# Kernel optimization log

Hardware: AMD Instinct MI355X
Metric: run time of the kernel (lower is better)

The kernel has to match this reference:

```python
import jax, jax.numpy as jnp
import numpy as np

D_ATTN = 2048
D_STATE = 64
SHIFT_FRAC = 0.5
LN_EPS = 1e-5


def setup_inputs() -> dict:
    key = jax.random.key(0)
    ks = jax.random.split(key, 8)
    B, T = 8, 2048
    s_attn = 1.0 / np.sqrt(D_ATTN)
    s_state = 1.0 / np.sqrt(D_STATE)
    x = jax.random.normal(ks[0], (B, T, D_ATTN), jnp.float32)
    W_key = jax.random.normal(ks[1], (D_STATE, D_ATTN), jnp.float32) * s_attn
    W_value = jax.random.normal(ks[2], (D_STATE, D_ATTN), jnp.float32) * s_attn
    W_output = jax.random.normal(ks[3], (D_ATTN, D_STATE), jnp.float32) * s_state
    W_shift = jax.random.normal(ks[4], (D_ATTN, D_ATTN), jnp.float32) * s_attn
    gate = jnp.ones((D_ATTN,), jnp.float32)
    # negative decay log so w = exp(time_decay) in (e^-1, 1): stable over T=2048 steps
    time_decay = -jax.random.uniform(ks[5], (D_STATE,), jnp.float32, 0.05, 1.0)
    time_first = jax.random.normal(ks[6], (D_STATE,), jnp.float32) * 0.1
    ln_gamma = jnp.ones((D_ATTN,), jnp.float32)
    ln_beta = jnp.zeros((D_ATTN,), jnp.float32)
    return dict(x=x, W_key=W_key, W_value=W_value, W_output=W_output,
                W_shift=W_shift, gate=gate, time_decay=time_decay,
                time_first=time_first, ln_gamma=ln_gamma, ln_beta=ln_beta)


def reference(x, W_key, W_value, W_output, W_shift, gate, time_decay,
              time_first, ln_gamma, ln_beta):
    B, T, D = x.shape
    # token shift: cat([x[:, s:], x[:, :-s]], dim=1) == roll(x, -s, axis=1)
    shift_len = max(1, int(T * SHIFT_FRAC))
    x_cat = jnp.roll(x, -shift_len, axis=1)
    g = jax.nn.sigmoid(gate)
    x_shift = jnp.einsum('btd,ed->bte', x_cat, W_shift) * g + x * (1.0 - g)
    # LayerNorm over last dim
    mu = jnp.mean(x_shift, axis=-1, keepdims=True)
    var = jnp.var(x_shift, axis=-1, keepdims=True)
    x_norm = (x_shift - mu) * jax.lax.rsqrt(var + LN_EPS) * ln_gamma + ln_beta
    k = jnp.einsum('btd,sd->bts', x_norm, W_key)    # (B,T,Ds)
    v = jnp.einsum('btd,sd->bts', x_norm, W_value)  # (B,T,Ds)
    w = jnp.exp(time_decay)                          # (Ds,)
    u = jnp.exp(time_first)                          # (Ds,)
    wkv = jnp.exp(-u * jax.nn.sigmoid(k)) * v        # (B,T,Ds)
    # linear recurrence: state_t = w * state_{t-1} + wkv_t
    def step(state, wkv_t):
        state = state * w + wkv_t
        return state, state
    init = jnp.zeros((B, k.shape[-1]), x.dtype)
    last_state, states = jax.lax.scan(step, init, jnp.swapaxes(wkv, 0, 1))
    states = jnp.swapaxes(states, 0, 1)              # (B,T,Ds)
    # per-step output projection == single batched GEMM over stacked states
    output = jnp.einsum('bts,ds->btd', states, W_output)  # (B,T,D)
    # dropout in eval mode is identity; last_state is detached in original
    return output, jax.lax.stop_gradient(last_state)
```

## Files before the change

kernel.cpp:

```cpp
#include <hip/hip_runtime.h>
#include <stdint.h>

constexpr int kD  = 2048;
constexpr int kDS = 64;
constexpr int kNT = 2048;
constexpr int kM  = 8 * kNT;
constexpr int kOutElems = kM * kD;

typedef __attribute__((ext_vector_type(8))) short short8;
typedef __attribute__((ext_vector_type(8))) unsigned short bfu8;
typedef __attribute__((ext_vector_type(4))) unsigned short bfu4;
typedef __attribute__((ext_vector_type(4))) float f32x4;

__device__ __forceinline__ unsigned short f2bf(float f) {
  unsigned int u = __float_as_uint(f);
  return (unsigned short)((u + 0x7FFFu + ((u >> 16) & 1u)) >> 16);
}
__device__ __forceinline__ float bf2f(unsigned short b) {
  return __uint_as_float(((unsigned int)b) << 16);
}

__device__ __forceinline__ void gload16(const void* g, void* l) {
  __builtin_amdgcn_global_load_lds((__attribute__((address_space(1))) void*)g,
                                   (__attribute__((address_space(3))) void*)l,
                                   16, 0, 0);
}

__global__ void k_cvt(const float* __restrict__ src, unsigned short* __restrict__ dst, int n8) {
  int i8 = blockIdx.x * 256 + threadIdx.x;
  if (i8 >= n8) return;
  const f32x4* s = (const f32x4*)(src + (size_t)i8 * 8);
  f32x4 v0 = s[0], v1 = s[1];
  bfu8 o;
  o[0] = f2bf(v0[0]); o[1] = f2bf(v0[1]); o[2] = f2bf(v0[2]); o[3] = f2bf(v0[3]);
  o[4] = f2bf(v1[0]); o[5] = f2bf(v1[1]); o[6] = f2bf(v1[2]); o[7] = f2bf(v1[3]);
  *(bfu8*)(dst + (size_t)i8 * 8) = o;
}

__global__ void k_cvt_kv(const float* __restrict__ wk, const float* __restrict__ wv,
                         unsigned short* __restrict__ dst) {
  int i8 = blockIdx.x * 256 + threadIdx.x;
  int r = i8 >> 8;
  int dcol = (i8 & 255) << 3;
  int s = r >> 1;
  const float* src = (r & 1) ? wv : wk;
  const f32x4* p = (const f32x4*)(src + (size_t)s * kD + dcol);
  f32x4 v0 = p[0], v1 = p[1];
  bfu8 o;
  o[0] = f2bf(v0[0]); o[1] = f2bf(v0[1]); o[2] = f2bf(v0[2]); o[3] = f2bf(v0[3]);
  o[4] = f2bf(v1[0]); o[5] = f2bf(v1[1]); o[6] = f2bf(v1[2]); o[7] = f2bf(v1[3]);
  *(bfu8*)(dst + (size_t)i8 * 8) = o;
}

#define MM(x,y,z) __builtin_amdgcn_mfma_f32_16x16x32_bf16(x,y,z,0,0,0)
#define BAR __builtin_amdgcn_s_barrier()
#define WAITV_(N) asm volatile("s_waitcnt vmcnt(" #N ")" ::: "memory")
#define WAITV(N) WAITV_(N)
#define WAITL asm volatile("s_waitcnt lgkmcnt(0)")
#define NOWV (void)0

#define STAGEA_TO(BUF,H,Q,KT) gload16(aS + (size_t)(((H)*64+(Q)*128)*2048) + (KT), \
                                      smem + (BUF)*32768 + ((H)*64+(Q)*128)*64 + ldsAst)
#define STAGEB_TO(BUF,H,Q,KT) gload16(bS + (size_t)(((H)*32+(Q)*128)*2048) + (KT), \
                                      smem + (BUF)*32768 + 16384 + (H)*2048 + (Q)*8192 + ldsBst)

#define RDA(CUR,H,MF,KS) (*(const short8*)(smem + (CUR)*32768 + ardb + (H)*4096 + (MF)*1024 + colrd##KS))
#define RDB(CUR,H,NF,KS) (*(const short8*)(smem + (CUR)*32768 + 16384 + brdb + (H)*2048 + (NF)*1024 + colrd##KS))

#define RD_A(CUR,H) \
  a[0][0]=RDA(CUR,H,0,0); a[0][1]=RDA(CUR,H,0,1); \
  a[1][0]=RDA(CUR,H,1,0); a[1][1]=RDA(CUR,H,1,1); \
  a[2][0]=RDA(CUR,H,2,0); a[2][1]=RDA(CUR,H,2,1); \
  a[3][0]=RDA(CUR,H,3,0); a[3][1]=RDA(CUR,H,3,1)
#define RD_B(CUR,H,BV) \
  BV[0][0]=RDB(CUR,H,0,0); BV[0][1]=RDB(CUR,H,0,1); \
  BV[1][0]=RDB(CUR,H,1,0); BV[1][1]=RDB(CUR,H,1,1)

#define MF16(MH, B, NB) \
  __builtin_amdgcn_s_setprio(1); \
  acc[(MH)*4+0][(NB)+0] = MM(a[0][0], B[0][0], acc[(MH)*4+0][(NB)+0]); \
  acc[(MH)*4+0][(NB)+1] = MM(a[0][0], B[1][0], acc[(MH)*4+0][(NB)+1]); \
  acc[(MH)*4+1][(NB)+0] = MM(a[1][0], B[0][0], acc[(MH)*4+1][(NB)+0]); \
  acc[(MH)*4+1][(NB)+1] = MM(a[1][0], B[1][0], acc[(MH)*4+1][(NB)+1]); \
  acc[(MH)*4+2][(NB)+0] = MM(a[2][0], B[0][0], acc[(MH)*4+2][(NB)+0]); \
  acc[(MH)*4+2][(NB)+1] = MM(a[2][0], B[1][0], acc[(MH)*4+2][(NB)+1]); \
  acc[(MH)*4+3][(NB)+0] = MM(a[3][0], B[0][0], acc[(MH)*4+3][(NB)+0]); \
  acc[(MH)*4+3][(NB)+1] = MM(a[3][0], B[1][0], acc[(MH)*4+3][(NB)+1]); \
  acc[(MH)*4+0][(NB)+0] = MM(a[0][1], B[0][1], acc[(MH)*4+0][(NB)+0]); \
  acc[(MH)*4+0][(NB)+1] = MM(a[0][1], B[1][1], acc[(MH)*4+0][(NB)+1]); \
  acc[(MH)*4+1][(NB)+0] = MM(a[1][1], B[0][1], acc[(MH)*4+1][(NB)+0]); \
  acc[(MH)*4+1][(NB)+1] = MM(a[1][1], B[1][1], acc[(MH)*4+1][(NB)+1]); \
  acc[(MH)*4+2][(NB)+0] = MM(a[2][1], B[0][1], acc[(MH)*4+2][(NB)+0]); \
  acc[(MH)*4+2][(NB)+1] = MM(a[2][1], B[1][1], acc[(MH)*4+2][(NB)+1]); \
  acc[(MH)*4+3][(NB)+0] = MM(a[3][1], B[0][1], acc[(MH)*4+3][(NB)+0]); \
  acc[(MH)*4+3][(NB)+1] = MM(a[3][1], B[1][1], acc[(MH)*4+3][(NB)+1]); \
  __builtin_amdgcn_s_setprio(0)

#define PH0(CUR, S, KA1, WV) \
  BAR; WAITL; MF16(0, b0, 0); \
  RD_B(CUR,1,b1); \
  if (S) { STAGEA_TO((CUR)^1, 1, 0, KA1); STAGEA_TO((CUR)^1, 1, 1, KA1); } \
  WV

#define PH1(CUR, S, KT2, WV) \
  BAR; WAITL; MF16(0, b1, 2); \
  RD_A(CUR,1); \
  if (S) { STAGEA_TO(CUR, 0, 0, KT2); STAGEA_TO(CUR, 0, 1, KT2); } \
  WV

#define PH2(CUR, S, KT2, WV) \
  BAR; WAITL; MF16(1, b0, 0); \
  if (S) { STAGEB_TO(CUR, 0, 0, KT2); STAGEB_TO(CUR, 0, 1, KT2); } \
  WV

#define PH3(CUR, RDN, S, KT2, WV) \
  BAR; WAITL; MF16(1, b1, 2); \
  if (RDN) { RD_A((CUR)^1,0); RD_B((CUR)^1,0,b0); } \
  if (S) { STAGEB_TO(CUR, 1, 0, KT2); STAGEB_TO(CUR, 1, 1, KT2); } \
  WV

__global__ __launch_bounds__(512, 2)
void k_gemm_shift8(const unsigned short* __restrict__ A,
                   const unsigned short* __restrict__ Bw,
                   const float* __restrict__ gate,
                   unsigned short* __restrict__ out) {
  __shared__ __align__(16) unsigned char smem_raw[131072];
  unsigned short* smem = (unsigned short*)smem_raw;

  const int tid = threadIdx.x;
  const int lane = tid & 63;
  const int w = tid >> 6;
  const int wr = w >> 2, wc = w & 3;
  const int lr = lane & 15, lq = lane >> 4;
  const int bid = blockIdx.x;
  const int nblk = bid & 7, mblk = bid >> 3;
  const int m0 = mblk * 256, n0 = nblk * 256;

  const int r0 = tid >> 3;
  const int colel = ((tid & 7) * 8) ^ (((tid >> 3) & 7) << 3);
  const unsigned short* aS = A + (size_t)((m0 ^ 1024) + r0) * 2048 + colel;
  const unsigned short* bS = Bw + (size_t)(n0 + ((tid >> 8) << 6) + (r0 & 31)) * 2048 + colel;
  const int ldsAst = tid * 8;
  const int ldsBst = ((tid >> 8) << 12) + (tid & 255) * 8;

  const int ardb = (wr * 128 + lr) * 64;
  const int brdb = (wc * 64 + lr) * 64;
  const int colrd0 = (lq * 8) ^ ((lr & 7) << 3);
  const int colrd1 = (32 + lq * 8) ^ ((lr & 7) << 3);

  short8 a[4][2], b0[2][2], b1[2][2];
  f32x4 acc[8][4] = {};

  STAGEA_TO(0,0,0,0); STAGEA_TO(0,0,1,0);
  STAGEB_TO(0,0,0,0); STAGEB_TO(0,0,1,0);
  STAGEB_TO(0,1,0,0); STAGEB_TO(0,1,1,0);
  STAGEA_TO(0,1,0,0); STAGEA_TO(0,1,1,0);
  STAGEA_TO(1,0,0,64); STAGEA_TO(1,0,1,64);
  STAGEB_TO(1,0,0,64); STAGEB_TO(1,0,1,64);
  STAGEB_TO(1,1,0,64); STAGEB_TO(1,1,1,64);
  WAITV(6); BAR;
  RD_A(0,0); RD_B(0,0,b0);

  int ka1 = 64, kt2 = 128;
  for (int j = 0; j < 15; ++j) {
    PH0(0, 1, ka1, WAITV(8)); PH1(0, 1, kt2, WAITV(8));
    PH2(0, 1, kt2, WAITV(8)); PH3(0, 1, 1, kt2, WAITV(8));
    ka1 += 64; kt2 += 64;
    PH0(1, 1, ka1, WAITV(8)); PH1(1, 1, kt2, WAITV(8));
    PH2(1, 1, kt2, WAITV(8)); PH3(1, 1, 1, kt2, WAITV(8));
    ka1 += 64; kt2 += 64;
  }
  PH0(0, 1, 1984, WAITV(8)); PH1(0, 0, 0, NOWV);
  PH2(0, 0, 0, WAITV(4));    PH3(0, 1, 0, 0, WAITV(2));
  PH0(1, 0, 0, WAITV(0));    PH1(1, 0, 0, NOWV);
  PH2(1, 0, 0, NOWV);        PH3(1, 0, 0, 0, NOWV);

  float* cbuf = (float*)smem_raw;
#pragma unroll
  for (int q = 0; q < 4; ++q) {
    __syncthreads();
    if (wr == (q >> 1)) {
#pragma unroll
      for (int mm = 0; mm < 4; ++mm) {
#pragma unroll
        for (int nf = 0; nf < 4; ++nf) {
#pragma unroll
          for (int i = 0; i < 4; ++i) {
            int rl = mm * 16 + lq * 4 + i;
            int cl = wc * 64 + nf * 16 + lr;
            cbuf[rl * 260 + cl] = acc[(q & 1) * 4 + mm][nf][i];
          }
        }
      }
    }
    __syncthreads();
#pragma unroll
    for (int it = 0; it < 4; ++it) {
      int idx = tid + it * 512;
      int rl = idx >> 5, cb = (idx & 31) * 8;
      int gr = m0 + q * 64 + rl, gc = n0 + cb;
      f32x4 c0 = *(const f32x4*)&cbuf[rl * 260 + cb];
      f32x4 c1 = *(const f32x4*)&cbuf[rl * 260 + cb + 4];
      f32x4 g0 = *(const f32x4*)&gate[gc];
      f32x4 g1 = *(const f32x4*)&gate[gc + 4];
      bfu8 xv = *(const bfu8*)(A + (size_t)gr * 2048 + gc);
      bfu8 o;
#pragma unroll
      for (int jj = 0; jj < 4; ++jj) {
        float g = 1.f / (1.f + __expf(-g0[jj]));
        o[jj] = f2bf(c0[jj] * g + bf2f(xv[jj]) * (1.f - g));
        float h = 1.f / (1.f + __expf(-g1[jj]));
        o[jj + 4] = f2bf(c1[jj] * h + bf2f(xv[jj + 4]) * (1.f - h));
      }
      *(bfu8*)(out + (size_t)gr * 2048 + gc) = o;
    }
  }
}

__launch_bounds__(256)
__global__ void k_ln(const unsigned short* __restrict__ xs, const float* __restrict__ gamma,
                     const float* __restrict__ beta, unsigned short* __restrict__ xn) {
  int m = blockIdx.x;
  int tid = threadIdx.x;
  bfu8 v = *(const bfu8*)(xs + (size_t)m * kD + tid * 8);
  float f[8];
#pragma unroll
  for (int j = 0; j < 8; ++j) f[j] = bf2f(v[j]);
  float s = 0.f, q = 0.f;
#pragma unroll
  for (int j = 0; j < 8; ++j) { s += f[j]; q += f[j] * f[j]; }
#pragma unroll
  for (int d = 1; d < 64; d <<= 1) { s += __shfl_xor(s, d); q += __shfl_xor(q, d); }
  __shared__ float ss[4], qq[4];
  if ((tid & 63) == 0) { ss[tid >> 6] = s; qq[tid >> 6] = q; }
  __syncthreads();
  s = ss[0] + ss[1] + ss[2] + ss[3];
  q = qq[0] + qq[1] + qq[2] + qq[3];
  float mean = s * (1.f / kD);
  float var = q * (1.f / kD) - mean * mean;
  float rstd = rsqrtf(var + 1e-5f);
  int d0 = tid * 8;
  bfu8 o;
#pragma unroll
  for (int j = 0; j < 8; ++j) {
    float g = gamma[d0 + j], b = beta[d0 + j];
    o[j] = f2bf((f[j] - mean) * rstd * g + b);
  }
  *(bfu8*)(xn + (size_t)m * kD + d0) = o;
}

__launch_bounds__(256, 2)
__global__ void k_gemm_kv(const unsigned short* __restrict__ A,
                          const unsigned short* __restrict__ Bw,
                          const float* __restrict__ tfirst,
                          float* __restrict__ wkv) {
  __shared__ __align__(16) unsigned short As[32 * 32];
  __shared__ __align__(16) unsigned short Bs[128 * 32];
  const int tid = threadIdx.x;
  const int lane = tid & 63;
  const int wcv = tid >> 6;
  const int m0 = blockIdx.x * 32;
  const int lr = lane & 15, lk = (lane >> 4) << 3;
  const int c1 = tid, c2 = tid + 256;

  const unsigned short* ga = A + (size_t)(m0 + (tid >> 2)) * kD + ((tid & 3) << 3);
  const unsigned short* gb0 = Bw + (size_t)(c1 >> 2) * kD + ((c1 & 3) << 3);
  const unsigned short* gb1 = Bw + (size_t)(c2 >> 2) * kD + ((c2 & 3) << 3);
  unsigned short* la = As + tid * 8;
  unsigned short* lb0 = Bs + c1 * 8;
  unsigned short* lb1 = Bs + c2 * 8;

  f32x4 acc[2][2] = {};

  for (int kt = 0; kt < kD; kt += 32) {
    __syncthreads();
    if (tid < 128) gload16(ga + kt, la);
    gload16(gb0 + kt, lb0);
    gload16(gb1 + kt, lb1);
    __syncthreads();
    short8 af[2], bf[2];
#pragma unroll
    for (int mf = 0; mf < 2; ++mf)
      af[mf] = *(const short8*)&As[(mf * 16 + lr) * 32 + lk];
#pragma unroll
    for (int nf = 0; nf < 2; ++nf)
      bf[nf] = *(const short8*)&Bs[(wcv * 32 + nf * 16 + lr) * 32 + lk];
#pragma unroll
    for (int mf = 0; mf < 2; ++mf)
#pragma unroll
      for (int nf = 0; nf < 2; ++nf)
        acc[mf][nf] = __builtin_amdgcn_mfma_f32_16x16x32_bf16(af[mf], bf[nf], acc[mf][nf], 0, 0, 0);
  }

  const int fq = lane >> 4, fr = lane & 15;
#pragma unroll
  for (int mf = 0; mf < 2; ++mf) {
#pragma unroll
    for (int nf = 0; nf < 2; ++nf) {
      int c = wcv * 32 + nf * 16 + fr;
#pragma unroll
      for (int i = 0; i < 4; ++i) {
        int r = m0 + mf * 16 + fq * 4 + i;
        float val = acc[mf][nf][i];
        float other = __shfl_xor(val, 1);
        if (!(c & 1)) {
          int s = c >> 1;
          float sk = 1.f / (1.f + expf(-val));
          float u = expf(tfirst[s]);
          wkv[(size_t)r * kDS + s] = expf(-u * sk) * other;
        }
      }
    }
  }
}

__global__ void k_scan(const float* __restrict__ wkv, const float* __restrict__ tdec,
                       float* __restrict__ states, float* __restrict__ last_state) {
  int chunk = blockIdx.x;
  int b = blockIdx.y;
  int s = threadIdx.x;
  float w = expf(tdec[s]);
  int t1 = chunk * 64;
  int warm = t1 < 256 ? t1 : 256;
  const float* base = wkv + (size_t)b * kNT * kDS + s;
  float* sbase = states + (size_t)b * kNT * kDS + s;
  float st = 0.f;
#pragma unroll 4
  for (int t = t1 - warm; t < t1; ++t) st = fmaf(st, w, base[(size_t)t * kDS]);
#pragma unroll 4
  for (int t = t1; t < t1 + 64; ++t) {
    st = fmaf(st, w, base[(size_t)t * kDS]);
    sbase[(size_t)t * kDS] = st;
  }
  if (chunk == 31) last_state[b * kDS + s] = st;
}

__launch_bounds__(256, 3)
__global__ void k_out_gemm(const float* __restrict__ states, const float* __restrict__ Wo,
                           float* __restrict__ out) {
  __shared__ float St[64 * 68];
  __shared__ float Wt[64 * 132];
  const int m0 = blockIdx.y * 64;
  const int n0 = blockIdx.x * 128;
  const int tid = threadIdx.x;
#pragma unroll
  for (int it = 0; it < 16; ++it) {
    int idx = tid + it * 256;
    int r = idx >> 6, s = idx & 63;
    St[s * 68 + r] = states[(size_t)(m0 + r) * kDS + s];
  }
#pragma unroll
  for (int it = 0; it < 32; ++it) {
    int idx = tid + it * 256;
    int dl = idx >> 6, s = idx & 63;
    Wt[s * 132 + dl] = Wo[(size_t)(n0 + dl) * kDS + s];
  }
  __syncthreads();
  const int pr = tid & 15, pc = tid >> 4;
  float acc[4][8] = {};
  for (int s = 0; s < 64; ++s) {
    f32x4 sv = *(const f32x4*)&St[s * 68 + pr * 4];
    f32x4 w0 = *(const f32x4*)&Wt[s * 132 + pc * 8];
    f32x4 w1 = *(const f32x4*)&Wt[s * 132 + pc * 8 + 4];
#pragma unroll
    for (int i = 0; i < 4; ++i) {
      float aa = sv[i];
#pragma unroll
      for (int j = 0; j < 4; ++j) {
        acc[i][j] = fmaf(aa, w0[j], acc[i][j]);
        acc[i][j + 4] = fmaf(aa, w1[j], acc[i][j + 4]);
      }
    }
  }
#pragma unroll
  for (int i = 0; i < 4; ++i) {
    int r = m0 + pr * 4 + i;
    f32x4 o0 = {acc[i][0], acc[i][1], acc[i][2], acc[i][3]};
    f32x4 o1 = {acc[i][4], acc[i][5], acc[i][6], acc[i][7]};
    *(f32x4*)&out[(size_t)r * kD + n0 + pc * 8] = o0;
    *(f32x4*)&out[(size_t)r * kD + n0 + pc * 8 + 4] = o1;
  }
}

extern "C" void kernel_launch(void* const* d_in, const int* in_sizes, int n_in,
                              void* d_out, int out_size, void* d_ws, size_t ws_size,
                              hipStream_t stream) {
  const float* x    = (const float*)d_in[0];
  const float* Wk   = (const float*)d_in[1];
  const float* Wv   = (const float*)d_in[2];
  const float* Wo   = (const float*)d_in[3];
  const float* Wsh  = (const float*)d_in[4];
  const float* gate = (const float*)d_in[5];
  const float* tdec = (const float*)d_in[6];
  const float* tfir = (const float*)d_in[7];
  const float* lng  = (const float*)d_in[8];
  const float* lnb  = (const float*)d_in[9];
  float* out = (float*)d_out;
  char* ws = (char*)d_ws;

  unsigned short* xbf   = (unsigned short*)(ws);
  unsigned short* wshbf = (unsigned short*)(ws + 67108864);
  unsigned short* wkvbf = (unsigned short*)(ws + 75497472);
  float* wkvf           = (float*)(ws + 76021760);
  float* statesf        = (float*)(ws + 80216064);

  k_cvt<<<16384, 256, 0, stream>>>(x, xbf, 4194304);
  k_cvt<<<2048, 256, 0, stream>>>(Wsh, wshbf, 524288);
  k_cvt_kv<<<128, 256, 0, stream>>>(Wk, Wv, wkvbf);

  k_gemm_shift8<<<512, 512, 0, stream>>>(xbf, wshbf, gate, (unsigned short*)out);
  k_ln<<<16384, 256, 0, stream>>>((const unsigned short*)out, lng, lnb, xbf);
  k_gemm_kv<<<512, 256, 0, stream>>>(xbf, wkvbf, tfir, wkvf);
  k_scan<<<dim3(32, 8), 64, 0, stream>>>(wkvf, tdec, statesf, out + kOutElems);
  k_out_gemm<<<dim3(16, 256), 256, 0, stream>>>(statesf, Wo, out);
}
```

Measured before the change: 312.6 us.

## Run output projection GEMM on bf16 MFMA with bf16 states and weights

The scan now writes states as bf16, W_output is converted to bf16, and the output projection GEMM is rewritten to use MFMA 16x16x32 bf16 instructions. Tiles are loaded into swizzled LDS with global_load_lds, and results are staged through LDS for coalesced fp32 stores. Tiles grow to 128x128. This replaces FP32 FMA compute and halves the state read traffic, but adds precision loss on the states and an extra conversion launch. The kernel is mostly bound by writing the large fp32 output.

```diff
diff --git a/kernel.cpp b/kernel.cpp
--- a/kernel.cpp
+++ b/kernel.cpp
@@ -315,7 +315,7 @@
 }
 
 __global__ void k_scan(const float* __restrict__ wkv, const float* __restrict__ tdec,
-                       float* __restrict__ states, float* __restrict__ last_state) {
+                       unsigned short* __restrict__ states, float* __restrict__ last_state) {
   int chunk = blockIdx.x;
   int b = blockIdx.y;
   int s = threadIdx.x;
@@ -323,62 +323,83 @@
   int t1 = chunk * 64;
   int warm = t1 < 256 ? t1 : 256;
   const float* base = wkv + (size_t)b * kNT * kDS + s;
-  float* sbase = states + (size_t)b * kNT * kDS + s;
+  unsigned short* sbase = states + (size_t)b * kNT * kDS + s;
   float st = 0.f;
 #pragma unroll 4
   for (int t = t1 - warm; t < t1; ++t) st = fmaf(st, w, base[(size_t)t * kDS]);
 #pragma unroll 4
   for (int t = t1; t < t1 + 64; ++t) {
     st = fmaf(st, w, base[(size_t)t * kDS]);
-    sbase[(size_t)t * kDS] = st;
+    sbase[(size_t)t * kDS] = f2bf(st);
   }
   if (chunk == 31) last_state[b * kDS + s] = st;
 }
 
-__launch_bounds__(256, 3)
-__global__ void k_out_gemm(const float* __restrict__ states, const float* __restrict__ Wo,
+__launch_bounds__(256, 2)
+__global__ void k_out_gemm(const unsigned short* __restrict__ states,
+                           const unsigned short* __restrict__ Wo,
                            float* __restrict__ out) {
-  __shared__ float St[64 * 68];
-  __shared__ float Wt[64 * 132];
-  const int m0 = blockIdx.y * 64;
+  __shared__ __align__(16) unsigned short As[128 * 64];
+  __shared__ __align__(16) unsigned short Bs[128 * 64];
+  __shared__ float cbuf[64 * 132];
+  const int tid = threadIdx.x;
+  const int lane = tid & 63;
+  const int w = tid >> 6;
+  const int wr = w >> 1, wc = w & 1;
+  const int lr = lane & 15, lq = lane >> 4;
   const int n0 = blockIdx.x * 128;
-  const int tid = threadIdx.x;
-#pragma unroll
-  for (int it = 0; it < 16; ++it) {
-    int idx = tid + it * 256;
-    int r = idx >> 6, s = idx & 63;
-    St[s * 68 + r] = states[(size_t)(m0 + r) * kDS + s];
-  }
-#pragma unroll
-  for (int it = 0; it < 32; ++it) {
-    int idx = tid + it * 256;
-    int dl = idx >> 6, s = idx & 63;
-    Wt[s * 132 + dl] = Wo[(size_t)(n0 + dl) * kDS + s];
+  const int m0 = blockIdx.y * 128;
+
+  const int sr0 = tid >> 3;
+  const int scol = ((tid & 7) * 8) ^ (((tid >> 3) & 7) << 3);
+#pragma unroll
+  for (int rd = 0; rd < 4; ++rd) {
+    gload16(states + (size_t)(m0 + sr0 + rd * 32) * 64 + scol, As + tid * 8 + rd * 2048);
+    gload16(Wo + (size_t)(n0 + sr0 + rd * 32) * 64 + scol, Bs + tid * 8 + rd * 2048);
   }
   __syncthreads();
-  const int pr = tid & 15, pc = tid >> 4;
-  float acc[4][8] = {};
-  for (int s = 0; s < 64; ++s) {
-    f32x4 sv = *(const f32x4*)&St[s * 68 + pr * 4];
-    f32x4 w0 = *(const f32x4*)&Wt[s * 132 + pc * 8];
-    f32x4 w1 = *(const f32x4*)&Wt[s * 132 + pc * 8 + 4];
-#pragma unroll
-    for (int i = 0; i < 4; ++i) {
-      float aa = sv[i];
-#pragma unroll
-      for (int j = 0; j < 4; ++j) {
-        acc[i][j] = fmaf(aa, w0[j], acc[i][j]);
-        acc[i][j + 4] = fmaf(aa, w1[j], acc[i][j + 4]);
-      }
-    }
-  }
-#pragma unroll
-  for (int i = 0; i < 4; ++i) {
-    int r = m0 + pr * 4 + i;
-    f32x4 o0 = {acc[i][0], acc[i][1], acc[i][2], acc[i][3]};
-    f32x4 o1 = {acc[i][4], acc[i][5], acc[i][6], acc[i][7]};
-    *(f32x4*)&out[(size_t)r * kD + n0 + pc * 8] = o0;
-    *(f32x4*)&out[(size_t)r * kD + n0 + pc * 8 + 4] = o1;
+
+  short8 a[4][2], b[4][2];
+#pragma unroll
+  for (int mf = 0; mf < 4; ++mf) {
+#pragma unroll
+    for (int ks = 0; ks < 2; ++ks) {
+      int col = (ks * 32 + lq * 8) ^ ((lr & 7) << 3);
+      a[mf][ks] = *(const short8*)&As[(wr * 64 + mf * 16 + lr) * 64 + col];
+      b[mf][ks] = *(const short8*)&Bs[(wc * 64 + mf * 16 + lr) * 64 + col];
+    }
+  }
+  f32x4 acc[4][4] = {};
+#pragma unroll
+  for (int mf = 0; mf < 4; ++mf)
+#pragma unroll
+    for (int nf = 0; nf < 4; ++nf) {
+      acc[mf][nf] = __builtin_amdgcn_mfma_f32_16x16x32_bf16(a[mf][0], b[nf][0], acc[mf][nf], 0, 0, 0);
+      acc[mf][nf] = __builtin_amdgcn_mfma_f32_16x16x32_bf16(a[mf][1], b[nf][1], acc[mf][nf], 0, 0, 0);
+    }
+
+#pragma unroll
+  for (int q = 0; q < 2; ++q) {
+    __syncthreads();
+    if (wr == q) {
+#pragma unroll
+      for (int mf = 0; mf < 4; ++mf)
+#pragma unroll
+        for (int nf = 0; nf < 4; ++nf)
+#pragma unroll
+          for (int i = 0; i < 4; ++i) {
+            int rl = mf * 16 + lq * 4 + i;
+            int cl = wc * 64 + nf * 16 + lr;
+            cbuf[rl * 132 + cl] = acc[mf][nf][i];
+          }
+    }
+    __syncthreads();
+#pragma unroll
+    for (int it = 0; it < 8; ++it) {
+      int idx = tid + it * 256;
+      int rl = idx >> 5, cb = (idx & 31) * 4;
+      *(f32x4*)&out[(size_t)(m0 + q * 64 + rl) * kD + n0 + cb] = *(const f32x4*)&cbuf[rl * 132 + cb];
+    }
   }
 }
 
@@ -402,15 +423,17 @@
   unsigned short* wshbf = (unsigned short*)(ws + 67108864);
   unsigned short* wkvbf = (unsigned short*)(ws + 75497472);
   float* wkvf           = (float*)(ws + 76021760);
-  float* statesf        = (float*)(ws + 80216064);
+  unsigned short* stbf  = (unsigned short*)(ws + 80216064);
+  unsigned short* wobf  = (unsigned short*)(ws + 82313216);
 
   k_cvt<<<16384, 256, 0, stream>>>(x, xbf, 4194304);
   k_cvt<<<2048, 256, 0, stream>>>(Wsh, wshbf, 524288);
+  k_cvt<<<64, 256, 0, stream>>>(Wo, wobf, 16384);
   k_cvt_kv<<<128, 256, 0, stream>>>(Wk, Wv, wkvbf);
 
   k_gemm_shift8<<<512, 512, 0, stream>>>(xbf, wshbf, gate, (unsigned short*)out);
   k_ln<<<16384, 256, 0, stream>>>((const unsigned short*)out, lng, lnb, xbf);
   k_gemm_kv<<<512, 256, 0, stream>>>(xbf, wkvbf, tfir, wkvf);
-  k_scan<<<dim3(32, 8), 64, 0, stream>>>(wkvf, tdec, statesf, out + kOutElems);
-  k_out_gemm<<<dim3(16, 256), 256, 0, stream>>>(statesf, Wo, out);
-}
+  k_scan<<<dim3(32, 8), 64, 0, stream>>>(wkvf, tdec, stbf, out + kOutElems);
+  k_out_gemm<<<dim3(16, 128), 256, 0, stream>>>(stbf, wobf, out);
+}
```

After: 288.8 us. 7.6% less time.
